# Kernel tuning notes

Measured on AMD Instinct MI355X. Metric: run time of the kernel, lower is better.

Reference implementation:

```python
import jax, jax.numpy as jnp
import numpy as np

H = 8          # n_heads
M = 16         # max_dist
U = 512        # n_units
DH = U // H    # d_head
EPS = 1e-3     # keras LayerNormalization default epsilon
NEG = -2.0**32 + 1.0


def _rel_table(pe, T):
    # pe: [2M+1, DH]; returns [T, T, DH] with rel[i, j] = pe[clip(j - i, -M, M) + M]
    i = jnp.arange(T)
    idx = jnp.clip(i[None, :] - i[:, None], -M, M) + M
    return pe[idx]


def _split_heads(x):
    # [B, T, U] -> [H*B, T, DH]  (head-major, matching tf.concat(tf.split(x, H, 2), 0))
    B, T, _ = x.shape
    return x.reshape(B, T, H, DH).transpose(2, 0, 1, 3).reshape(H * B, T, DH)


def _merge_heads(x, B):
    # [H*B, T, DH] -> [B, T, U]
    T = x.shape[1]
    return x.reshape(H, B, T, DH).transpose(1, 2, 0, 3).reshape(B, T, U)


def setup_inputs() -> dict:
    key = jax.random.key(0)
    ks = jax.random.split(key, 10)
    B, T = 8, 1024
    s = 1.0 / np.sqrt(U)
    inp = {
        'q': jax.random.normal(ks[0], (B, T, U), jnp.float32),
        'k': jax.random.normal(ks[1], (B, T, U), jnp.float32),
        'v': jax.random.normal(ks[2], (B, T, U), jnp.float32),
        'Wq': jax.random.normal(ks[3], (U, U), jnp.float32) * s,
        'bq': jnp.zeros((U,), jnp.float32),
        'Wk': jax.random.normal(ks[4], (U, U), jnp.float32) * s,
        'bk': jnp.zeros((U,), jnp.float32),
        'Wv': jax.random.normal(ks[5], (U, U), jnp.float32) * s,
        'bv': jnp.zeros((U,), jnp.float32),
        'Wo': jax.random.normal(ks[6], (U, U), jnp.float32) * s,
        'bo': jnp.zeros((U,), jnp.float32),
        'gamma': jnp.ones((U,), jnp.float32),
        'beta': jnp.zeros((U,), jnp.float32),
        'pe_k': jax.random.normal(ks[7], (2 * M + 1, DH), jnp.float32) * 0.05,
        'pe_v': jax.random.normal(ks[8], (2 * M + 1, DH), jnp.float32) * 0.05,
    }
    return inp


def reference(q, k, v, Wq, bq, Wk, bk, Wv, bv, Wo, bo, gamma, beta, pe_k, pe_v):
    B, T, _ = q.shape
    relu = jax.nn.relu
    q_emb = relu(q @ Wq + bq)
    k_emb = relu(k @ Wk + bk)
    v_emb = relu(v @ Wv + bv)
    qh = _split_heads(q_emb)   # [HB, T, DH]
    kh = _split_heads(k_emb)
    vh = _split_heads(v_emb)

    attn = jnp.einsum('btd,bsd->bts', qh, kh)
    rel_k = _rel_table(pe_k, T)                       # [T, T, DH]
    attn = attn + jnp.einsum('btd,tsd->bts', qh, rel_k)
    attn = attn / jnp.asarray(DH, attn.dtype) ** 0.5

    causal = jnp.tril(jnp.ones((T, T), jnp.bool_))
    attn = jnp.where(causal[None], attn, jnp.asarray(NEG, attn.dtype))
    w = jax.nn.softmax(attn, axis=-1)

    out = jnp.einsum('bts,bsd->btd', w, vh)
    rel_v = _rel_table(pe_v, T)
    out = out + jnp.einsum('bts,tsd->btd', w, rel_v)

    out = _merge_heads(out, B)                        # [B, T, U]
    out = relu(out @ Wo + bo)
    out = out + q

    mu = jnp.mean(out, axis=-1, keepdims=True)
    var = jnp.mean(jnp.square(out - mu), axis=-1, keepdims=True)
    return (out - mu) * jax.lax.rsqrt(var + EPS) * gamma + beta
```

## Files before the change

### kernel.cpp

```cpp
#include <hip/hip_runtime.h>
#include <hip/hip_bf16.h>

#define T_SEQ 1024
#define U_DIM 512
#define LN_EPS 1e-3f

typedef float  f32x4  __attribute__((ext_vector_type(4)));
typedef short  bf16x8 __attribute__((ext_vector_type(8)));

__device__ __forceinline__ unsigned short f2bf(float f) {
    union { float f; unsigned u; } x; x.f = f;
    unsigned r = x.u + 0x7fffu + ((x.u >> 16) & 1u);
    return (unsigned short)(r >> 16);
}
__device__ __forceinline__ int packbf(float a, float b) {
    return (int)((unsigned)f2bf(a) | ((unsigned)f2bf(b) << 16));
}
__device__ __forceinline__ void async_copy16(void* lds, const void* g) {
    __builtin_amdgcn_global_load_lds((const __attribute__((address_space(1))) void*)g,
                                     (__attribute__((address_space(3))) void*)lds, 16, 0, 0);
}

__global__ __launch_bounds__(256) void prep_wt(const float* __restrict__ W0,
                                               const float* __restrict__ W1,
                                               const float* __restrict__ W2,
                                               const float* __restrict__ W3,
                                               short* __restrict__ wt) {
    __shared__ float Ws[64][65];
    const int z = blockIdx.z;
    const float* W = (z == 0) ? W0 : (z == 1) ? W1 : (z == 2) ? W2 : W3;
    short* Wt = wt + (size_t)z * 262144;
    const int k0 = blockIdx.x * 64, n0 = blockIdx.y * 64;
    const int t = threadIdx.x;
    {
        const int kr = t >> 2, cs = (t & 3) * 16;
        const float4* src = (const float4*)(W + (size_t)(k0 + kr) * 512 + n0 + cs);
#pragma unroll
        for (int i = 0; i < 4; ++i) {
            float4 v = src[i];
            Ws[kr][cs + 4 * i + 0] = v.x;
            Ws[kr][cs + 4 * i + 1] = v.y;
            Ws[kr][cs + 4 * i + 2] = v.z;
            Ws[kr][cs + 4 * i + 3] = v.w;
        }
    }
    __syncthreads();
    {
        const int nr = t >> 2, ks = (t & 3) * 16;
        int4 w0, w1;
        w0.x = packbf(Ws[ks + 0][nr], Ws[ks + 1][nr]);
        w0.y = packbf(Ws[ks + 2][nr], Ws[ks + 3][nr]);
        w0.z = packbf(Ws[ks + 4][nr], Ws[ks + 5][nr]);
        w0.w = packbf(Ws[ks + 6][nr], Ws[ks + 7][nr]);
        w1.x = packbf(Ws[ks + 8][nr], Ws[ks + 9][nr]);
        w1.y = packbf(Ws[ks + 10][nr], Ws[ks + 11][nr]);
        w1.z = packbf(Ws[ks + 12][nr], Ws[ks + 13][nr]);
        w1.w = packbf(Ws[ks + 14][nr], Ws[ks + 15][nr]);
        short* dst = Wt + (size_t)(n0 + nr) * 512 + k0 + ks;
        *(int4*)dst = w0;
        *(int4*)(dst + 8) = w1;
    }
}

template <int AFP32, int OUT>
__global__ __launch_bounds__(256) void gemm_mfma(
        const void* __restrict__ A0, const void* __restrict__ A1, const void* __restrict__ A2,
        const short* __restrict__ Wt0, const short* __restrict__ Wt1, const short* __restrict__ Wt2,
        const float* __restrict__ b0p, const float* __restrict__ b1p, const float* __restrict__ b2p,
        const float* __restrict__ resid,
        void* __restrict__ O0, void* __restrict__ O1, void* __restrict__ O2) {
    __shared__ short As[8192];
    __shared__ short Bs[8192];

    const int z = blockIdx.z;
    const void* Av = (z == 0) ? A0 : (z == 1) ? A1 : A2;
    const short* Wz = (z == 0) ? Wt0 : (z == 1) ? Wt1 : Wt2;
    const float* bz = (z == 0) ? b0p : (z == 1) ? b1p : b2p;
    void* Ov = (z == 0) ? O0 : (z == 1) ? O1 : O2;

    const int tid = threadIdx.x;
    const int m0 = blockIdx.x * 128, n0 = blockIdx.y * 128;
    const int w = tid >> 6, lane = tid & 63;
    const int n15 = lane & 15, g = lane >> 4;
    const int mh = w >> 1, nh = w & 1;

    f32x4 acc[4][4];
#pragma unroll
    for (int i = 0; i < 4; ++i)
#pragma unroll
        for (int j = 0; j < 4; ++j) acc[i][j] = (f32x4){0.f, 0.f, 0.f, 0.f};

    const int am = tid >> 1, akh = tid & 1;

    for (int ck = 0; ck < 8; ++ck) {
        const int k0 = ck * 64;
        if (ck) __syncthreads();

        if (AFP32) {
            const float* asrc = (const float*)Av + (size_t)(m0 + am) * 512 + k0 + akh * 32;
            float4 f[8];
#pragma unroll
            for (int i = 0; i < 8; ++i) f[i] = ((const float4*)asrc)[i];
            short* cell = As + (akh * 8 + (am >> 4)) * 512;
#pragma unroll
            for (int gg = 0; gg < 4; ++gg) {
                int4 wv;
                wv.x = packbf(f[2 * gg].x, f[2 * gg].y);
                wv.y = packbf(f[2 * gg].z, f[2 * gg].w);
                wv.z = packbf(f[2 * gg + 1].x, f[2 * gg + 1].y);
                wv.w = packbf(f[2 * gg + 1].z, f[2 * gg + 1].w);
                *(int4*)(cell + ((am & 15) + 16 * gg) * 8) = wv;
            }
            if (w < 2) {
#pragma unroll
                for (int i = 0; i < 8; ++i) {
                    const int kc = i >> 2, nt = w * 4 + (i & 3);
                    const short* gp = Wz + (size_t)(n0 + nt * 16 + n15) * 512 + k0 + kc * 32 + g * 8;
                    async_copy16(Bs + (kc * 8 + nt) * 512, gp);
                }
            }
        } else {
            if (w < 2) {
#pragma unroll
                for (int i = 0; i < 8; ++i) {
                    const int kc = i >> 2, nt = w * 4 + (i & 3);
                    const short* gp = Wz + (size_t)(n0 + nt * 16 + n15) * 512 + k0 + kc * 32 + g * 8;
                    async_copy16(Bs + (kc * 8 + nt) * 512, gp);
                }
            } else {
#pragma unroll
                for (int i = 0; i < 8; ++i) {
                    const int kc = i >> 2, mt = (w - 2) * 4 + (i & 3);
                    const short* gp = (const short*)Av + (size_t)(m0 + mt * 16 + n15) * 512 + k0 + kc * 32 + g * 8;
                    async_copy16(As + (kc * 8 + mt) * 512, gp);
                }
            }
        }
        __syncthreads();

#pragma unroll
        for (int kc = 0; kc < 2; ++kc) {
            bf16x8 af[4], bf[4];
#pragma unroll
            for (int i = 0; i < 4; ++i)
                af[i] = *(const bf16x8*)(As + (kc * 8 + mh * 4 + i) * 512 + lane * 8);
#pragma unroll
            for (int j = 0; j < 4; ++j)
                bf[j] = *(const bf16x8*)(Bs + (kc * 8 + nh * 4 + j) * 512 + lane * 8);
#pragma unroll
            for (int i = 0; i < 4; ++i)
#pragma unroll
                for (int j = 0; j < 4; ++j)
                    acc[i][j] = __builtin_amdgcn_mfma_f32_16x16x32_bf16(af[i], bf[j], acc[i][j], 0, 0, 0);
        }
    }

    const int mbase = m0 + mh * 64 + g * 4;
    const int nbase = n0 + nh * 64 + n15;
    const bool even = (n15 & 1) == 0;
    float bj[4];
#pragma unroll
    for (int j = 0; j < 4; ++j) bj[j] = bz[nbase + j * 16];

#pragma unroll
    for (int i = 0; i < 4; ++i) {
        const int mrow = mbase + i * 16;
#pragma unroll
        for (int j = 0; j < 4; ++j) {
            const int ncol = nbase + j * 16;
            f32x4 a = acc[i][j];
// ... 31 lines not shown
                    *(float2*)(Oz + (size_t)(mrow + 1) * 512 + ncol) = make_float2(v1 + r1.x, x1 + r1.y);
                } else {
                    float2 r2 = *(const float2*)(resid + (size_t)(mrow + 2) * 512 + ncol - 1);
                    float2 r3 = *(const float2*)(resid + (size_t)(mrow + 3) * 512 + ncol - 1);
                    *(float2*)(Oz + (size_t)(mrow + 2) * 512 + ncol - 1) = make_float2(x2 + r2.x, v2 + r2.y);
                    *(float2*)(Oz + (size_t)(mrow + 3) * 512 + ncol - 1) = make_float2(x3 + r3.x, v3 + r3.y);
                }
            }
        }
    }
}

__global__ __launch_bounds__(256) void attn_mfma(
        const short* __restrict__ qe, const short* __restrict__ ke,
        const short* __restrict__ ve, const float* __restrict__ pe_k,
        const float* __restrict__ pe_v, short* __restrict__ ao) {
    __shared__ short Ks[64 * 72];
    __shared__ short Vt[64 * 72];
    __shared__ float qpeS[128 * 17];
    __shared__ float wsumS[128 * 17];
    __shared__ float alphaS[128];
    __shared__ float lfinS[128];
    __shared__ float pevS[17 * 64];

    const int tid = threadIdx.x;
    const int qt = 7 - (int)blockIdx.x;
    const int hb = blockIdx.y;
    const int h = hb >> 3, b = hb & 7;
    const int t0 = qt * 128;
    const int w = tid >> 6;
    const int lane = tid & 63;
    const int g = lane >> 4;
    const int n15 = lane & 15;
    const int qbase = t0 + w * 32;

    float* qpeW  = qpeS  + w * (32 * 17);
    float* wsumW = wsumS + w * (32 * 17);
    float* alphaW = alphaS + w * 32;
    float* lW = lfinS + w * 32;

    for (int i = tid; i < 17 * 64; i += 256) pevS[i] = pe_v[i];

    bf16x8 Bq[2][2];
#pragma unroll
    for (int nt = 0; nt < 2; ++nt)
#pragma unroll
    for (int kh = 0; kh < 2; ++kh)
        Bq[nt][kh] = *(const bf16x8*)(qe + (size_t)(b * T_SEQ + qbase + nt * 16 + n15) * U_DIM
                                      + h * 64 + kh * 32 + g * 8);

    {
        f32x4 qa[2][2];
#pragma unroll
        for (int mt = 0; mt < 2; ++mt)
#pragma unroll
        for (int nt = 0; nt < 2; ++nt) qa[mt][nt] = (f32x4){0.f, 0.f, 0.f, 0.f};
#pragma unroll
        for (int mt = 0; mt < 2; ++mt)
#pragma unroll
        for (int kh = 0; kh < 2; ++kh) {
            const float* src = pe_k + (mt * 16 + n15) * 64 + kh * 32 + g * 8;
            float4 f0 = *(const float4*)src;
            float4 f1 = *(const float4*)(src + 4);
// ... 4 lines not shown
            fr[6] = (short)f2bf(f1.z); fr[7] = (short)f2bf(f1.w);
#pragma unroll
            for (int nt = 0; nt < 2; ++nt)
                qa[mt][nt] = __builtin_amdgcn_mfma_f32_16x16x32_bf16(fr, Bq[nt][kh], qa[mt][nt], 0, 0, 0);
        }
#pragma unroll
        for (int mt = 0; mt < 2; ++mt)
#pragma unroll
        for (int nt = 0; nt < 2; ++nt)
#pragma unroll
        for (int r = 0; r < 4; ++r) {
            const int ri = mt * 16 + 4 * g + r;
            if (ri <= 16) qpeW[(nt * 16 + n15) * 17 + ri] = qa[mt][nt][r];
        }
    }

    for (int i = lane; i < 32 * 17; i += 64) wsumW[i] = 0.f;

    float m_r[2] = {-3.0e38f, -3.0e38f};
    float l_r[2] = {0.f, 0.f};
    float b0[2]  = {0.f, 0.f};
    f32x4 oacc[2][4];
#pragma unroll
    for (int nt = 0; nt < 2; ++nt)
#pragma unroll
    for (int dt = 0; dt < 4; ++dt) oacc[nt][dt] = (f32x4){0.f, 0.f, 0.f, 0.f};

    const int wqhi = qbase + 31;
    const int send = t0 + 127;

    for (int s0 = 0; s0 <= send; s0 += 64) {
        __syncthreads();
        {
            const int sl = tid >> 2, dseg = (tid & 3) * 16;
            const short* src = ke + (size_t)(b * T_SEQ + s0 + sl) * U_DIM + h * 64 + dseg;
            *(int4*)(Ks + sl * 72 + dseg)     = *(const int4*)src;
            *(int4*)(Ks + sl * 72 + dseg + 8) = *(const int4*)(src + 8);
        }
        {
            const int sp = tid & 31, dbase = (tid >> 5) * 8;
            const short* r0 = ve + (size_t)(b * T_SEQ + s0 + 2 * sp) * U_DIM + h * 64 + dbase;
            const short* r1 = r0 + U_DIM;
            bf16x8 x8 = *(const bf16x8*)r0;
            bf16x8 y8 = *(const bf16x8*)r1;
#pragma unroll
            for (int i = 0; i < 8; ++i) {
                int pv = (int)((unsigned short)x8[i]) | (((int)(unsigned short)y8[i]) << 16);
                *(int*)(Vt + (dbase + i) * 72 + 2 * sp) = pv;
            }
        }
        __syncthreads();

        if (s0 > wqhi) continue;

        int cls[4][2];
#pragma unroll
        for (int mt = 0; mt < 4; ++mt)
#pragma unroll
        for (int nt = 0; nt < 2; ++nt) {
            const int slo = s0 + mt * 16;
            const int qlo = qbase + nt * 16;
            cls[mt][nt] = (slo > qlo + 15) ? 0 : ((slo + 31 < qlo) ? 1 : 2);
        }

        f32x4 c[4][2];
#pragma unroll
        for (int mt = 0; mt < 4; ++mt)
#pragma unroll
        for (int nt = 0; nt < 2; ++nt) c[mt][nt] = (f32x4){0.f, 0.f, 0.f, 0.f};
#pragma unroll
        for (int mt = 0; mt < 4; ++mt) {
            if (cls[mt][0] == 0 && cls[mt][1] == 0) continue;
#pragma unroll
            for (int kh = 0; kh < 2; ++kh) {
                bf16x8 ak = *(const bf16x8*)(Ks + (mt * 16 + n15) * 72 + kh * 32 + g * 8);
#pragma unroll
                for (int nt = 0; nt < 2; ++nt)
                    if (cls[mt][nt])
                        c[mt][nt] = __builtin_amdgcn_mfma_f32_16x16x32_bf16(ak, Bq[nt][kh], c[mt][nt], 0, 0, 0);
            }
        }

        float p[4][2][4];
        float alpha_l[2];
#pragma unroll
        for (int nt = 0; nt < 2; ++nt) {
            const int qg = qbase + nt * 16 + n15;
            const float qpe0 = qpeW[(nt * 16 + n15) * 17];
            float sc[4][4];
            float pmax = -3.0e38f;
#pragma unroll
            for (int mt = 0; mt < 4; ++mt) {
                if (cls[mt][nt] == 0) {
#pragma unroll
                    for (int r = 0; r < 4; ++r) sc[mt][r] = -3.0e38f;
                } else if (cls[mt][nt] == 1) {
#pragma unroll
                    for (int r = 0; r < 4; ++r) {
                        sc[mt][r] = (c[mt][nt][r] + qpe0) * 0.125f;
                        pmax = fmaxf(pmax, sc[mt][r]);
                    }
                } else {
#pragma unroll
                    for (int r = 0; r < 4; ++r) {
                        const int sg = s0 + mt * 16 + 4 * g + r;
                        const int dlt = sg - qg;
                        if (dlt <= 0) {
                            const int ri = (dlt < -16) ? 0 : (dlt + 16);
                            sc[mt][r] = (c[mt][nt][r] + qpeW[(nt * 16 + n15) * 17 + ri]) * 0.125f;
                            pmax = fmaxf(pmax, sc[mt][r]);
                        } else {
                            sc[mt][r] = -3.0e38f;
                        }
                    }
                }
            }
            pmax = fmaxf(pmax, __shfl_xor(pmax, 16, 64));
            pmax = fmaxf(pmax, __shfl_xor(pmax, 32, 64));
            const float mnew = fmaxf(m_r[nt], pmax);
            const float alpha = __expf(m_r[nt] - mnew);
            float psum = 0.f;
#pragma unroll
            for (int mt = 0; mt < 4; ++mt)
#pragma unroll
            for (int r = 0; r < 4; ++r) {
                const float pv = (cls[mt][nt] == 0) ? 0.f : __expf(sc[mt][r] - mnew);
                p[mt][nt][r] = pv;
                psum += pv;
            }
            psum += __shfl_xor(psum, 16, 64);
            psum += __shfl_xor(psum, 32, 64);
            l_r[nt] = l_r[nt] * alpha + psum;
            m_r[nt] = mnew;
            alpha_l[nt] = alpha;
            b0[nt] *= alpha;
        }

        if (g == 0) { alphaW[n15] = alpha_l[0]; alphaW[16 + n15] = alpha_l[1]; }
        for (int i = lane; i < 544; i += 64) wsumW[i] *= alphaW[i / 17];
#pragma unroll
        for (int nt = 0; nt < 2; ++nt) {
            const int qg = qbase + nt * 16 + n15;
#pragma unroll
            for (int mt = 0; mt < 4; ++mt) {
                if (cls[mt][nt] == 1) {
                    b0[nt] += p[mt][nt][0] + p[mt][nt][1] + p[mt][nt][2] + p[mt][nt][3];
                } else if (cls[mt][nt] == 2) {
#pragma unroll
                    for (int r = 0; r < 4; ++r) {
                        const int sg = s0 + mt * 16 + 4 * g + r;
                        const int dlt = sg - qg;
                        if (dlt <= 0) {
                            if (dlt >= -16)
                                atomicAdd(&wsumW[(nt * 16 + n15) * 17 + dlt + 16], p[mt][nt][r]);
                            else
                                b0[nt] += p[mt][nt][r];
                        }
                    }
                }
            }
        }

        int pk01[4][2], pk23[4][2];
#pragma unroll
        for (int mt = 0; mt < 4; ++mt)
#pragma unroll
        for (int nt = 0; nt < 2; ++nt) {
            pk01[mt][nt] = packbf(p[mt][nt][0], p[mt][nt][1]);
            pk23[mt][nt] = packbf(p[mt][nt][2], p[mt][nt][3]);
        }
        const int srcA = ((g & 1) * 2) * 16 + n15;
        const int srcB = srcA + 16;
        const bool selHi = (g >> 1) != 0;
#pragma unroll
        for (int nt = 0; nt < 2; ++nt) {
            float aO[4];
#pragma unroll
            for (int r = 0; r < 4; ++r) aO[r] = alphaW[nt * 16 + 4 * g + r];
#pragma unroll
            for (int dt = 0; dt < 4; ++dt)
#pragma unroll
            for (int r = 0; r < 4; ++r) oacc[nt][dt][r] *= aO[r];
#pragma unroll
            for (int kh = 0; kh < 2; ++kh) {
                if (cls[2 * kh][nt] == 0 && cls[2 * kh + 1][nt] == 0) continue;
                const int a0l = __shfl(pk01[2 * kh][nt], srcA, 64);
                const int a0h = __shfl(pk01[2 * kh + 1][nt], srcA, 64);
                const int a1l = __shfl(pk23[2 * kh][nt], srcA, 64);
                const int a1h = __shfl(pk23[2 * kh + 1][nt], srcA, 64);
                const int a2l = __shfl(pk01[2 * kh][nt], srcB, 64);
                const int a2h = __shfl(pk01[2 * kh + 1][nt], srcB, 64);
                const int a3l = __shfl(pk23[2 * kh][nt], srcB, 64);
                const int a3h = __shfl(pk23[2 * kh + 1][nt], srcB, 64);
                union { int i[4]; bf16x8 v; } au;
                au.i[0] = selHi ? a0h : a0l;
                au.i[1] = selHi ? a1h : a1l;
                au.i[2] = selHi ? a2h : a2l;
                au.i[3] = selHi ? a3h : a3l;
#pragma unroll
                for (int dt = 0; dt < 4; ++dt) {
                    bf16x8 bv = *(const bf16x8*)(Vt + (dt * 16 + n15) * 72 + kh * 32 + g * 8);
                    oacc[nt][dt] = __builtin_amdgcn_mfma_f32_16x16x32_bf16(au.v, bv, oacc[nt][dt], 0, 0, 0);
                }
            }
        }
    }

#pragma unroll
    for (int nt = 0; nt < 2; ++nt) {
        float t = b0[nt];
        t += __shfl_xor(t, 16, 64);
        t += __shfl_xor(t, 32, 64);
        if (g == 0) wsumW[(nt * 16 + n15) * 17] += t;
    }
    if (g == 0) { lW[n15] = l_r[0]; lW[16 + n15] = l_r[1]; }

#pragma unroll
    for (int nt = 0; nt < 2; ++nt)
#pragma unroll
    for (int r = 0; r < 4; ++r) {
        const int ql = nt * 16 + 4 * g + r;
        const int qg = qbase + ql;
        const float linv = 1.0f / lW[ql];
        float w17[17];
#pragma unroll
        for (int ri = 0; ri < 17; ++ri) w17[ri] = wsumW[ql * 17 + ri];
        short* dst = ao + (size_t)(b * T_SEQ + qg) * U_DIM + h * 64 + n15;
#pragma unroll
        for (int dt = 0; dt < 4; ++dt) {
            float relv = 0.f;
#pragma unroll
            for (int ri = 0; ri < 17; ++ri) relv += w17[ri] * pevS[ri * 64 + dt * 16 + n15];
            dst[dt * 16] = (short)f2bf((oacc[nt][dt][r] + relv) * linv);
        }
    }
}

__global__ __launch_bounds__(256) void ln_kernel(float* __restrict__ io,
                                                 const float* __restrict__ gamma,
                                                 const float* __restrict__ beta) {
    const int row = blockIdx.x;
    const int tid = threadIdx.x;
    float* rp = &io[(size_t)row * 512];
    float2 v = *(float2*)&rp[tid * 2];

    float s = v.x + v.y;
#pragma unroll
    for (int off = 32; off > 0; off >>= 1) s += __shfl_down(s, off);

    __shared__ float red[4];
    __shared__ float bc[2];
    const int wid = tid >> 6, lane = tid & 63;
    if (lane == 0) red[wid] = s;
    __syncthreads();
    if (tid == 0) bc[0] = (red[0] + red[1] + red[2] + red[3]) * (1.0f / 512.0f);
    __syncthreads();
    const float mu = bc[0];

    const float d0 = v.x - mu, d1 = v.y - mu;
    float sq = d0 * d0 + d1 * d1;
#pragma unroll
    for (int off = 32; off > 0; off >>= 1) sq += __shfl_down(sq, off);
    if (lane == 0) red[wid] = sq;
    __syncthreads();
    if (tid == 0)
        bc[1] = rsqrtf((red[0] + red[1] + red[2] + red[3]) * (1.0f / 512.0f) + LN_EPS);
    __syncthreads();
    const float rs = bc[1];

    const int c = tid * 2;
    float2 o;
    o.x = d0 * rs * gamma[c] + beta[c];
    o.y = d1 * rs * gamma[c + 1] + beta[c + 1];
    *(float2*)&rp[c] = o;
}

extern "C" void kernel_launch(void* const* d_in, const int* in_sizes, int n_in,
                              void* d_out, int out_size, void* d_ws, size_t ws_size,
                              hipStream_t stream) {
    const float* q     = (const float*)d_in[0];
    const float* k     = (const float*)d_in[1];
    const float* v     = (const float*)d_in[2];
    const float* Wq    = (const float*)d_in[3];
    const float* bq    = (const float*)d_in[4];
    const float* Wk    = (const float*)d_in[5];
    const float* bk    = (const float*)d_in[6];
    const float* Wv    = (const float*)d_in[7];
    const float* bv    = (const float*)d_in[8];
    const float* Wo    = (const float*)d_in[9];
    const float* bo    = (const float*)d_in[10];
    const float* gamma = (const float*)d_in[11];
    const float* beta  = (const float*)d_in[12];
    const float* pe_k  = (const float*)d_in[13];
    const float* pe_v  = (const float*)d_in[14];
    float* out = (float*)d_out;

    char* base = (char*)d_ws;
    short* qe = (short*)(base);
    short* ke = (short*)(base + (((size_t)8) << 20));
    short* ve = (short*)(base + (((size_t)16) << 20));
    short* ao = (short*)(base + (((size_t)24) << 20));
    short* wt = (short*)(base + (((size_t)32) << 20));
    short* wtq = wt, *wtk = wt + 262144, *wtv = wt + 2 * 262144, *wto = wt + 3 * 262144;

    prep_wt<<<dim3(8, 8, 4), 256, 0, stream>>>(Wq, Wk, Wv, Wo, wt);
    gemm_mfma<1, 0><<<dim3(64, 4, 3), 256, 0, stream>>>(
        q, k, v, wtq, wtk, wtv, bq, bk, bv, nullptr, qe, ke, ve);
    attn_mfma<<<dim3(8, 64), 256, 0, stream>>>(qe, ke, ve, pe_k, pe_v, ao);
    gemm_mfma<0, 1><<<dim3(64, 4, 1), 256, 0, stream>>>(
        ao, ao, ao, wto, wto, wto, bo, bo, bo, q, out, out, out);
    ln_kernel<<<dim3(8192), 256, 0, stream>>>(out, gamma, beta);
}
```

Measured before the change: 282.2 us.

## Restructure pipeline: bf16 pre-cast, double-buffered GEMM, split band rel-v kernel, warp LN

After: 273.1 us. 1.03x faster.

```diff
diff --git a/kernel.cpp b/kernel.cpp
--- a/kernel.cpp
+++ b/kernel.cpp
@@ -13,6 +13,10 @@
     unsigned r = x.u + 0x7fffu + ((x.u >> 16) & 1u);
     return (unsigned short)(r >> 16);
 }
+__device__ __forceinline__ float b2f(short s) {
+    union { unsigned u; float f; } x; x.u = ((unsigned)(unsigned short)s) << 16;
+    return x.f;
+}
 __device__ __forceinline__ int packbf(float a, float b) {
     return (int)((unsigned)f2bf(a) | ((unsigned)f2bf(b) << 16));
 }
@@ -21,59 +25,79 @@
                                      (__attribute__((address_space(3))) void*)lds, 16, 0, 0);
 }
 
-__global__ __launch_bounds__(256) void prep_wt(const float* __restrict__ W0,
-                                               const float* __restrict__ W1,
-                                               const float* __restrict__ W2,
-                                               const float* __restrict__ W3,
-                                               short* __restrict__ wt) {
+__global__ __launch_bounds__(256) void prep_all(
+        const float* __restrict__ Wq, const float* __restrict__ Wk,
+        const float* __restrict__ Wv, const float* __restrict__ Wo,
+        short* __restrict__ wt,
+        const float* __restrict__ q, const float* __restrict__ k,
+        const float* __restrict__ v,
+        short* __restrict__ qb, short* __restrict__ kb, short* __restrict__ vb) {
     __shared__ float Ws[64][65];
-    const int z = blockIdx.z;
-    const float* W = (z == 0) ? W0 : (z == 1) ? W1 : (z == 2) ? W2 : W3;
-    short* Wt = wt + (size_t)z * 262144;
-    const int k0 = blockIdx.x * 64, n0 = blockIdx.y * 64;
-    const int t = threadIdx.x;
-    {
-        const int kr = t >> 2, cs = (t & 3) * 16;
-        const float4* src = (const float4*)(W + (size_t)(k0 + kr) * 512 + n0 + cs);
-#pragma unroll
-        for (int i = 0; i < 4; ++i) {
-            float4 v = src[i];
-            Ws[kr][cs + 4 * i + 0] = v.x;
-            Ws[kr][cs + 4 * i + 1] = v.y;
-            Ws[kr][cs + 4 * i + 2] = v.z;
-            Ws[kr][cs + 4 * i + 3] = v.w;
-        }
-    }
-    __syncthreads();
-    {
-        const int nr = t >> 2, ks = (t & 3) * 16;
-        int4 w0, w1;
-        w0.x = packbf(Ws[ks + 0][nr], Ws[ks + 1][nr]);
-        w0.y = packbf(Ws[ks + 2][nr], Ws[ks + 3][nr]);
-        w0.z = packbf(Ws[ks + 4][nr], Ws[ks + 5][nr]);
-        w0.w = packbf(Ws[ks + 6][nr], Ws[ks + 7][nr]);
-        w1.x = packbf(Ws[ks + 8][nr], Ws[ks + 9][nr]);
-        w1.y = packbf(Ws[ks + 10][nr], Ws[ks + 11][nr]);
-        w1.z = packbf(Ws[ks + 12][nr], Ws[ks + 13][nr]);
-        w1.w = packbf(Ws[ks + 14][nr], Ws[ks + 15][nr]);
-        short* dst = Wt + (size_t)(n0 + nr) * 512 + k0 + ks;
-        *(int4*)dst = w0;
-        *(int4*)(dst + 8) = w1;
-    }
-}
-
-template <int AFP32, int OUT>
-__global__ __launch_bounds__(256) void gemm_mfma(
-        const void* __restrict__ A0, const void* __restrict__ A1, const void* __restrict__ A2,
+    const int bid = blockIdx.x, t = threadIdx.x;
+    if (bid < 256) {
+        const int z = bid >> 6, tile = bid & 63;
+        const float* W = (z == 0) ? Wq : (z == 1) ? Wk : (z == 2) ? Wv : Wo;
+        short* Wt = wt + (size_t)z * 262144;
+        const int k0 = (tile >> 3) * 64, n0 = (tile & 7) * 64;
+        {
+            const int kr = t >> 2, cs = (t & 3) * 16;
+            const float4* src = (const float4*)(W + (size_t)(k0 + kr) * 512 + n0 + cs);
+#pragma unroll
+            for (int i = 0; i < 4; ++i) {
+                float4 vv = src[i];
+                Ws[kr][cs + 4 * i + 0] = vv.x;
+                Ws[kr][cs + 4 * i + 1] = vv.y;
+                Ws[kr][cs + 4 * i + 2] = vv.z;
+                Ws[kr][cs + 4 * i + 3] = vv.w;
+            }
+        }
+        __syncthreads();
+        {
+            const int nr = t >> 2, ks = (t & 3) * 16;
+            int4 w0, w1;
+            w0.x = packbf(Ws[ks + 0][nr], Ws[ks + 1][nr]);
+            w0.y = packbf(Ws[ks + 2][nr], Ws[ks + 3][nr]);
+            w0.z = packbf(Ws[ks + 4][nr], Ws[ks + 5][nr]);
+            w0.w = packbf(Ws[ks + 6][nr], Ws[ks + 7][nr]);
+            w1.x = packbf(Ws[ks + 8][nr], Ws[ks + 9][nr]);
+            w1.y = packbf(Ws[ks + 10][nr], Ws[ks + 11][nr]);
+            w1.z = packbf(Ws[ks + 12][nr], Ws[ks + 13][nr]);
+            w1.w = packbf(Ws[ks + 14][nr], Ws[ks + 15][nr]);
+            short* dst = Wt + (size_t)(n0 + nr) * 512 + k0 + ks;
+            *(int4*)dst = w0;
+            *(int4*)(dst + 8) = w1;
+        }
+    } else {
+        const int aid = bid - 256;
+        const int tsr = aid >> 10, chunk = aid & 1023;
+        const float* src = ((tsr == 0) ? q : (tsr == 1) ? k : v) + (size_t)chunk * 4096 + t * 16;
+        short* dst = ((tsr == 0) ? qb : (tsr == 1) ? kb : vb) + (size_t)chunk * 4096 + t * 16;
+        float4 f0 = ((const float4*)src)[0];
+        float4 f1 = ((const float4*)src)[1];
+        float4 f2 = ((const float4*)src)[2];
+        float4 f3 = ((const float4*)src)[3];
+        int4 o0, o1;
+        o0.x = packbf(f0.x, f0.y); o0.y = packbf(f0.z, f0.w);
+        o0.z = packbf(f1.x, f1.y); o0.w = packbf(f1.z, f1.w);
+        o1.x = packbf(f2.x, f2.y); o1.y = packbf(f2.z, f2.w);
+        o1.z = packbf(f3.x, f3.y); o1.w = packbf(f3.z, f3.w);
+        *(int4*)dst = o0;
+        *(int4*)(dst + 8) = o1;
+    }
+}
+
+template <int OUT>
+__global__ __launch_bounds__(256) void gemm_bf16(
+        const short* __restrict__ A0, const short* __restrict__ A1, const short* __restrict__ A2,
         const short* __restrict__ Wt0, const short* __restrict__ Wt1, const short* __restrict__ Wt2,
         const float* __restrict__ b0p, const float* __restrict__ b1p, const float* __restrict__ b2p,
         const float* __restrict__ resid,
         void* __restrict__ O0, void* __restrict__ O1, void* __restrict__ O2) {
-    __shared__ short As[8192];
-    __shared__ short Bs[8192];
+    __shared__ short As[2 * 8192];
+    __shared__ short Bs[2 * 8192];
 
     const int z = blockIdx.z;
-    const void* Av = (z == 0) ? A0 : (z == 1) ? A1 : A2;
+    const short* Az = (z == 0) ? A0 : (z == 1) ? A1 : A2;
     const short* Wz = (z == 0) ? Wt0 : (z == 1) ? Wt1 : Wt2;
     const float* bz = (z == 0) ? b0p : (z == 1) ? b1p : b2p;
     void* Ov = (z == 0) ? O0 : (z == 1) ? O1 : O2;
@@ -90,70 +114,50 @@
 #pragma unroll
         for (int j = 0; j < 4; ++j) acc[i][j] = (f32x4){0.f, 0.f, 0.f, 0.f};
 
-    const int am = tid >> 1, akh = tid & 1;
-
+#define GEMM_STAGE(CK, BUF)                                                              \
+    do {                                                                                 \
+        const int k0s = (CK) * 64;                                                       \
+        short* Ab = As + (BUF) * 8192;                                                   \
+        short* Bb = Bs + (BUF) * 8192;                                                   \
+        if (w < 2) {                                                                     \
+            _Pragma("unroll")                                                            \
+            for (int i = 0; i < 8; ++i) {                                                \
+                const int kc = i >> 2, nt = w * 4 + (i & 3);                             \
+                const short* gp = Wz + (size_t)(n0 + nt * 16 + n15) * 512 + k0s + kc * 32 + g * 8; \
+                async_copy16(Bb + (kc * 8 + nt) * 512, gp);                              \
+            }                                                                            \
+        } else {                                                                         \
+            _Pragma("unroll")                                                            \
+            for (int i = 0; i < 8; ++i) {                                                \
+                const int kc = i >> 2, mt = (w - 2) * 4 + (i & 3);                       \
+                const short* gp = Az + (size_t)(m0 + mt * 16 + n15) * 512 + k0s + kc * 32 + g * 8; \
+                async_copy16(Ab + (kc * 8 + mt) * 512, gp);                              \
+            }                                                                            \
+        }                                                                                \
+    } while (0)
+
+    GEMM_STAGE(0, 0);
     for (int ck = 0; ck < 8; ++ck) {
-        const int k0 = ck * 64;
-        if (ck) __syncthreads();
-
-        if (AFP32) {
-            const float* asrc = (const float*)Av + (size_t)(m0 + am) * 512 + k0 + akh * 32;
-            float4 f[8];
-#pragma unroll
-            for (int i = 0; i < 8; ++i) f[i] = ((const float4*)asrc)[i];
-            short* cell = As + (akh * 8 + (am >> 4)) * 512;
-#pragma unroll
-            for (int gg = 0; gg < 4; ++gg) {
-                int4 wv;
-                wv.x = packbf(f[2 * gg].x, f[2 * gg].y);
-                wv.y = packbf(f[2 * gg].z, f[2 * gg].w);
-                wv.z = packbf(f[2 * gg + 1].x, f[2 * gg + 1].y);
-                wv.w = packbf(f[2 * gg + 1].z, f[2 * gg + 1].w);
-                *(int4*)(cell + ((am & 15) + 16 * gg) * 8) = wv;
-            }
-            if (w < 2) {
-#pragma unroll
-                for (int i = 0; i < 8; ++i) {
-                    const int kc = i >> 2, nt = w * 4 + (i & 3);
-                    const short* gp = Wz + (size_t)(n0 + nt * 16 + n15) * 512 + k0 + kc * 32 + g * 8;
-                    async_copy16(Bs + (kc * 8 + nt) * 512, gp);
-                }
-            }
-        } else {
-            if (w < 2) {
-#pragma unroll
-                for (int i = 0; i < 8; ++i) {
-                    const int kc = i >> 2, nt = w * 4 + (i & 3);
-                    const short* gp = Wz + (size_t)(n0 + nt * 16 + n15) * 512 + k0 + kc * 32 + g * 8;
-                    async_copy16(Bs + (kc * 8 + nt) * 512, gp);
-                }
-            } else {
-#pragma unroll
-                for (int i = 0; i < 8; ++i) {
-                    const int kc = i >> 2, mt = (w - 2) * 4 + (i & 3);
-                    const short* gp = (const short*)Av + (size_t)(m0 + mt * 16 + n15) * 512 + k0 + kc * 32 + g * 8;
-                    async_copy16(As + (kc * 8 + mt) * 512, gp);
-                }
-            }
-        }
         __syncthreads();
-
+        if (ck < 7) GEMM_STAGE(ck + 1, (ck + 1) & 1);
+        const int buf = ck & 1;
 #pragma unroll
         for (int kc = 0; kc < 2; ++kc) {
-            bf16x8 af[4], bf[4];
+            bf16x8 af[4], bfv[4];
 #pragma unroll
             for (int i = 0; i < 4; ++i)
-                af[i] = *(const bf16x8*)(As + (kc * 8 + mh * 4 + i) * 512 + lane * 8);
+                af[i] = *(const bf16x8*)(As + buf * 8192 + (kc * 8 + mh * 4 + i) * 512 + lane * 8);
 #pragma unroll
             for (int j = 0; j < 4; ++j)
-                bf[j] = *(const bf16x8*)(Bs + (kc * 8 + nh * 4 + j) * 512 + lane * 8);
+                bfv[j] = *(const bf16x8*)(Bs + buf * 8192 + (kc * 8 + nh * 4 + j) * 512 + lane * 8);
 #pragma unroll
             for (int i = 0; i < 4; ++i)
 #pragma unroll
                 for (int j = 0; j < 4; ++j)
-                    acc[i][j] = __builtin_amdgcn_mfma_f32_16x16x32_bf16(af[i], bf[j], acc[i][j], 0, 0, 0);
-        }
-    }
+                    acc[i][j] = __builtin_amdgcn_mfma_f32_16x16x32_bf16(af[i], bfv[j], acc[i][j], 0, 0, 0);
+        }
+    }
+#undef GEMM_STAGE
 
     const int mbase = m0 + mh * 64 + g * 4;
     const int nbase = n0 + nh * 64 + n15;
@@ -215,39 +219,31 @@
 __global__ __launch_bounds__(256) void attn_mfma(
         const short* __restrict__ qe, const short* __restrict__ ke,
         const short* __restrict__ ve, const float* __restrict__ pe_k,
-        const float* __restrict__ pe_v, short* __restrict__ ao) {
-    __shared__ short Ks[64 * 72];
-    __shared__ short Vt[64 * 72];
-    __shared__ float qpeS[128 * 17];
-    __shared__ float wsumS[128 * 17];
-    __shared__ float alphaS[128];
-    __shared__ float lfinS[128];
-    __shared__ float pevS[17 * 64];
+        float* __restrict__ ml, short* __restrict__ ao) {
+    __shared__ short Kc[2 * 4096];
+    __shared__ short Vt[2 * 4608];
+    __shared__ float qpeS[4 * 32 * 17];
 
     const int tid = threadIdx.x;
     const int qt = 7 - (int)blockIdx.x;
     const int hb = blockIdx.y;
     const int h = hb >> 3, b = hb & 7;
     const int t0 = qt * 128;
-    const int w = tid >> 6;
-    const int lane = tid & 63;
-    const int g = lane >> 4;
-    const int n15 = lane & 15;
-    const int qbase = t0 + w * 32;
-
-    float* qpeW  = qpeS  + w * (32 * 17);
-    float* wsumW = wsumS + w * (32 * 17);
-    float* alphaW = alphaS + w * 32;
-    float* lW = lfinS + w * 32;
-
-    for (int i = tid; i < 17 * 64; i += 256) pevS[i] = pe_v[i];
+    const int w = tid >> 6, lane = tid & 63;
+    const int g = lane >> 4, n15 = lane & 15;
+    const int qn[2] = {t0 + w * 16, t0 + (7 - w) * 16};
+    const int wqhi = qn[1] + 15;
+    const int nsteps = (t0 + 128) >> 6;
+    const int sp = tid & 31, dbase = (tid >> 5) * 8;
+
+    float* qpeW = qpeS + w * (32 * 17);
 
     bf16x8 Bq[2][2];
 #pragma unroll
     for (int nt = 0; nt < 2; ++nt)
 #pragma unroll
     for (int kh = 0; kh < 2; ++kh)
-        Bq[nt][kh] = *(const bf16x8*)(qe + (size_t)(b * T_SEQ + qbase + nt * 16 + n15) * U_DIM
+        Bq[nt][kh] = *(const bf16x8*)(qe + (size_t)(b * T_SEQ + qn[nt] + n15) * U_DIM
                                       + h * 64 + kh * 32 + g * 8);
 
     {
@@ -282,265 +278,328 @@
             if (ri <= 16) qpeW[(nt * 16 + n15) * 17 + ri] = qa[mt][nt][r];
         }
     }
-
-    for (int i = lane; i < 32 * 17; i += 64) wsumW[i] = 0.f;
+    const float qpe0r[2] = { qpeW[(n15) * 17], qpeW[(16 + n15) * 17] };
 
     float m_r[2] = {-3.0e38f, -3.0e38f};
     float l_r[2] = {0.f, 0.f};
-    float b0[2]  = {0.f, 0.f};
     f32x4 oacc[2][4];
 #pragma unroll
     for (int nt = 0; nt < 2; ++nt)
 #pragma unroll
     for (int dt = 0; dt < 4; ++dt) oacc[nt][dt] = (f32x4){0.f, 0.f, 0.f, 0.f};
 
-    const int wqhi = qbase + 31;
-    const int send = t0 + 127;
-
-    for (int s0 = 0; s0 <= send; s0 += 64) {
+    {
+#pragma unroll
+        for (int j = 0; j < 2; ++j) {
+            const int cc = 2 * w + j, kh = cc >> 2, mt = cc & 3;
+            const short* gp = ke + (size_t)(b * T_SEQ + mt * 16 + n15) * U_DIM + h * 64 + kh * 32 + g * 8;
+            async_copy16(Kc + cc * 512, gp);
+        }
+        const short* r0 = ve + (size_t)(b * T_SEQ + 2 * sp) * U_DIM + h * 64 + dbase;
+        bf16x8 vx = *(const bf16x8*)r0, vy = *(const bf16x8*)(r0 + U_DIM);
+#pragma unroll
+        for (int ii = 0; ii < 8; ++ii) {
+            int pv = (int)((unsigned short)vx[ii]) | (((int)(unsigned short)vy[ii]) << 16);
+            *(int*)(Vt + (dbase + ii) * 72 + 2 * sp) = pv;
+        }
+    }
+
+    for (int i = 0; i < nsteps; ++i) {
+        const int s0 = i << 6;
+        const int cbuf = i & 1, nbuf = cbuf ^ 1;
+        const bool hasnext = (i + 1) < nsteps;
+        bf16x8 vx, vy;
         __syncthreads();
-        {
-            const int sl = tid >> 2, dseg = (tid & 3) * 16;
-            const short* src = ke + (size_t)(b * T_SEQ + s0 + sl) * U_DIM + h * 64 + dseg;
-            *(int4*)(Ks + sl * 72 + dseg)     = *(const int4*)src;
-            *(int4*)(Ks + sl * 72 + dseg + 8) = *(const int4*)(src + 8);
-        }
-        {
-            const int sp = tid & 31, dbase = (tid >> 5) * 8;
-            const short* r0 = ve + (size_t)(b * T_SEQ + s0 + 2 * sp) * U_DIM + h * 64 + dbase;
-            const short* r1 = r0 + U_DIM;
-            bf16x8 x8 = *(const bf16x8*)r0;
-            bf16x8 y8 = *(const bf16x8*)r1;
-#pragma unroll
-            for (int i = 0; i < 8; ++i) {
-                int pv = (int)((unsigned short)x8[i]) | (((int)(unsigned short)y8[i]) << 16);
-                *(int*)(Vt + (dbase + i) * 72 + 2 * sp) = pv;
-            }
-        }
-        __syncthreads();
-
-        if (s0 > wqhi) continue;
-
-        int cls[4][2];
-#pragma unroll
-        for (int mt = 0; mt < 4; ++mt)
-#pragma unroll
-        for (int nt = 0; nt < 2; ++nt) {
-            const int slo = s0 + mt * 16;
-            const int qlo = qbase + nt * 16;
-            cls[mt][nt] = (slo > qlo + 15) ? 0 : ((slo + 31 < qlo) ? 1 : 2);
-        }
-
-        f32x4 c[4][2];
-#pragma unroll
-        for (int mt = 0; mt < 4; ++mt)
-#pragma unroll
-        for (int nt = 0; nt < 2; ++nt) c[mt][nt] = (f32x4){0.f, 0.f, 0.f, 0.f};
-#pragma unroll
-        for (int mt = 0; mt < 4; ++mt) {
-            if (cls[mt][0] == 0 && cls[mt][1] == 0) continue;
-#pragma unroll
-            for (int kh = 0; kh < 2; ++kh) {
-                bf16x8 ak = *(const bf16x8*)(Ks + (mt * 16 + n15) * 72 + kh * 32 + g * 8);
-#pragma unroll
-                for (int nt = 0; nt < 2; ++nt)
-                    if (cls[mt][nt])
-                        c[mt][nt] = __builtin_amdgcn_mfma_f32_16x16x32_bf16(ak, Bq[nt][kh], c[mt][nt], 0, 0, 0);
-            }
-        }
-
-        float p[4][2][4];
-        float alpha_l[2];
-#pragma unroll
-        for (int nt = 0; nt < 2; ++nt) {
-            const int qg = qbase + nt * 16 + n15;
-            const float qpe0 = qpeW[(nt * 16 + n15) * 17];
-            float sc[4][4];
-            float pmax = -3.0e38f;
+        if (hasnext) {
+            const int sn = s0 + 64;
+#pragma unroll
+            for (int j = 0; j < 2; ++j) {
+                const int cc = 2 * w + j, kh = cc >> 2, mt = cc & 3;
+                const short* gp = ke + (size_t)(b * T_SEQ + sn + mt * 16 + n15) * U_DIM + h * 64 + kh * 32 + g * 8;
+                async_copy16(Kc + nbuf * 4096 + cc * 512, gp);
+            }
+            const short* r0 = ve + (size_t)(b * T_SEQ + sn + 2 * sp) * U_DIM + h * 64 + dbase;
+            vx = *(const bf16x8*)r0;
+            vy = *(const bf16x8*)(r0 + U_DIM);
+        }
+
+        if (s0 <= wqhi) {
+            int cls[4][2];
+#pragma unroll
+            for (int mt = 0; mt < 4; ++mt)
+#pragma unroll
+            for (int nt = 0; nt < 2; ++nt) {
+                const int slo = s0 + mt * 16;
+                const int qlo = qn[nt];
+                cls[mt][nt] = (slo > qlo + 15) ? 0 : ((slo + 31 < qlo) ? 1 : 2);
+            }
+
+            f32x4 c[4][2];
+#pragma unroll
+            for (int mt = 0; mt < 4; ++mt)
+#pragma unroll
+            for (int nt = 0; nt < 2; ++nt) c[mt][nt] = (f32x4){0.f, 0.f, 0.f, 0.f};
 #pragma unroll
             for (int mt = 0; mt < 4; ++mt) {
-                if (cls[mt][nt] == 0) {
-#pragma unroll
-                    for (int r = 0; r < 4; ++r) sc[mt][r] = -3.0e38f;
-                } else if (cls[mt][nt] == 1) {
-#pragma unroll
-                    for (int r = 0; r < 4; ++r) {
-                        sc[mt][r] = (c[mt][nt][r] + qpe0) * 0.125f;
-                        pmax = fmaxf(pmax, sc[mt][r]);
-                    }
-                } else {
-#pragma unroll
-                    for (int r = 0; r < 4; ++r) {
-                        const int sg = s0 + mt * 16 + 4 * g + r;
-                        const int dlt = sg - qg;
-                        if (dlt <= 0) {
-                            const int ri = (dlt < -16) ? 0 : (dlt + 16);
-                            sc[mt][r] = (c[mt][nt][r] + qpeW[(nt * 16 + n15) * 17 + ri]) * 0.125f;
+                if (cls[mt][0] == 0 && cls[mt][1] == 0) continue;
+#pragma unroll
+                for (int kh = 0; kh < 2; ++kh) {
+                    bf16x8 ak = *(const bf16x8*)(Kc + cbuf * 4096 + (kh * 4 + mt) * 512 + lane * 8);
+#pragma unroll
+                    for (int nt = 0; nt < 2; ++nt)
+                        if (cls[mt][nt])
+                            c[mt][nt] = __builtin_amdgcn_mfma_f32_16x16x32_bf16(ak, Bq[nt][kh], c[mt][nt], 0, 0, 0);
+                }
+            }
+
+            float p[4][2][4];
+            float alpha_l[2];
+#pragma unroll
+            for (int nt = 0; nt < 2; ++nt) {
+                const int qg = qn[nt] + n15;
+                float sc[4][4];
+                float pmax = -3.0e38f;
+#pragma unroll
+                for (int mt = 0; mt < 4; ++mt) {
+                    if (cls[mt][nt] == 0) {
+#pragma unroll
+                        for (int r = 0; r < 4; ++r) sc[mt][r] = -3.0e38f;
+                    } else if (cls[mt][nt] == 1) {
+#pragma unroll
+                        for (int r = 0; r < 4; ++r) {
+                            sc[mt][r] = (c[mt][nt][r] + qpe0r[nt]) * 0.125f;
                             pmax = fmaxf(pmax, sc[mt][r]);
-                        } else {
-                            sc[mt][r] = -3.0e38f;
+                        }
+                    } else {
+#pragma unroll
+                        for (int r = 0; r < 4; ++r) {
+                            const int sg = s0 + mt * 16 + 4 * g + r;
+                            const int dlt = sg - qg;
+                            if (dlt <= 0) {
+                                const int ri = (dlt < -16) ? 0 : (dlt + 16);
+                                sc[mt][r] = (c[mt][nt][r] + qpeW[(nt * 16 + n15) * 17 + ri]) * 0.125f;
+                                pmax = fmaxf(pmax, sc[mt][r]);
+                            } else {
+                                sc[mt][r] = -3.0e38f;
+                            }
                         }
                     }
                 }
-            }
-            pmax = fmaxf(pmax, __shfl_xor(pmax, 16, 64));
-            pmax = fmaxf(pmax, __shfl_xor(pmax, 32, 64));
-            const float mnew = fmaxf(m_r[nt], pmax);
-            const float alpha = __expf(m_r[nt] - mnew);
-            float psum = 0.f;
+                pmax = fmaxf(pmax, __shfl_xor(pmax, 16, 64));
+                pmax = fmaxf(pmax, __shfl_xor(pmax, 32, 64));
+                const float mnew = fmaxf(m_r[nt], pmax);
+                const float alpha = __expf(m_r[nt] - mnew);
+                float psum = 0.f;
+#pragma unroll
+                for (int mt = 0; mt < 4; ++mt)
+#pragma unroll
+                for (int r = 0; r < 4; ++r) {
+                    const float pv = (cls[mt][nt] == 0) ? 0.f : __expf(sc[mt][r] - mnew);
+                    p[mt][nt][r] = pv;
+                    psum += pv;
+                }
+                psum += __shfl_xor(psum, 16, 64);
+                psum += __shfl_xor(psum, 32, 64);
+                l_r[nt] = l_r[nt] * alpha + psum;
+                m_r[nt] = mnew;
+                alpha_l[nt] = alpha;
+            }
+
+            int pk01[4][2], pk23[4][2];
 #pragma unroll
             for (int mt = 0; mt < 4; ++mt)
 #pragma unroll
-            for (int r = 0; r < 4; ++r) {
-                const float pv = (cls[mt][nt] == 0) ? 0.f : __expf(sc[mt][r] - mnew);
-                p[mt][nt][r] = pv;
-                psum += pv;
-            }
-            psum += __shfl_xor(psum, 16, 64);
-            psum += __shfl_xor(psum, 32, 64);
-            l_r[nt] = l_r[nt] * alpha + psum;
-            m_r[nt] = mnew;
-            alpha_l[nt] = alpha;
-            b0[nt] *= alpha;
-        }
-
-        if (g == 0) { alphaW[n15] = alpha_l[0]; alphaW[16 + n15] = alpha_l[1]; }
-        for (int i = lane; i < 544; i += 64) wsumW[i] *= alphaW[i / 17];
-#pragma unroll
-        for (int nt = 0; nt < 2; ++nt) {
-            const int qg = qbase + nt * 16 + n15;
-#pragma unroll
-            for (int mt = 0; mt < 4; ++mt) {
-                if (cls[mt][nt] == 1) {
-                    b0[nt] += p[mt][nt][0] + p[mt][nt][1] + p[mt][nt][2] + p[mt][nt][3];
-                } else if (cls[mt][nt] == 2) {
-#pragma unroll
-                    for (int r = 0; r < 4; ++r) {
-                        const int sg = s0 + mt * 16 + 4 * g + r;
-                        const int dlt = sg - qg;
-                        if (dlt <= 0) {
-                            if (dlt >= -16)
-                                atomicAdd(&wsumW[(nt * 16 + n15) * 17 + dlt + 16], p[mt][nt][r]);
-                            else
-                                b0[nt] += p[mt][nt][r];
-                        }
+            for (int nt = 0; nt < 2; ++nt) {
+                pk01[mt][nt] = packbf(p[mt][nt][0], p[mt][nt][1]);
+                pk23[mt][nt] = packbf(p[mt][nt][2], p[mt][nt][3]);
+            }
+            const int srcA = ((g & 1) * 2) * 16 + n15;
+            const int srcB = srcA + 16;
+            const bool selHi = (g >> 1) != 0;
+#pragma unroll
+            for (int nt = 0; nt < 2; ++nt) {
+                float aO[4];
+#pragma unroll
+                for (int r = 0; r < 4; ++r) aO[r] = __shfl(alpha_l[nt], 4 * g + r, 64);
+#pragma unroll
+                for (int dt = 0; dt < 4; ++dt)
+#pragma unroll
+                for (int r = 0; r < 4; ++r) oacc[nt][dt][r] *= aO[r];
+#pragma unroll
+                for (int kh = 0; kh < 2; ++kh) {
+                    if (cls[2 * kh][nt] == 0 && cls[2 * kh + 1][nt] == 0) continue;
+                    const int a0l = __shfl(pk01[2 * kh][nt], srcA, 64);
+                    const int a0h = __shfl(pk01[2 * kh + 1][nt], srcA, 64);
+                    const int a1l = __shfl(pk23[2 * kh][nt], srcA, 64);
+                    const int a1h = __shfl(pk23[2 * kh + 1][nt], srcA, 64);
+                    const int a2l = __shfl(pk01[2 * kh][nt], srcB, 64);
+                    const int a2h = __shfl(pk01[2 * kh + 1][nt], srcB, 64);
+                    const int a3l = __shfl(pk23[2 * kh][nt], srcB, 64);
+                    const int a3h = __shfl(pk23[2 * kh + 1][nt], srcB, 64);
+                    union { int i[4]; bf16x8 v; } au;
+                    au.i[0] = selHi ? a0h : a0l;
+                    au.i[1] = selHi ? a1h : a1l;
+                    au.i[2] = selHi ? a2h : a2l;
+                    au.i[3] = selHi ? a3h : a3l;
+#pragma unroll
+                    for (int dt = 0; dt < 4; ++dt) {
+                        bf16x8 bv = *(const bf16x8*)(Vt + cbuf * 4608 + (dt * 16 + n15) * 72 + kh * 32 + g * 8);
+                        oacc[nt][dt] = __builtin_amdgcn_mfma_f32_16x16x32_bf16(au.v, bv, oacc[nt][dt], 0, 0, 0);
                     }
                 }
             }
         }
 
-        int pk01[4][2], pk23[4][2];
-#pragma unroll
-        for (int mt = 0; mt < 4; ++mt)
-#pragma unroll
-        for (int nt = 0; nt < 2; ++nt) {
-            pk01[mt][nt] = packbf(p[mt][nt][0], p[mt][nt][1]);
-            pk23[mt][nt] = packbf(p[mt][nt][2], p[mt][nt][3]);
-        }
-        const int srcA = ((g & 1) * 2) * 16 + n15;
-        const int srcB = srcA + 16;
-        const bool selHi = (g >> 1) != 0;
-#pragma unroll
-        for (int nt = 0; nt < 2; ++nt) {
-            float aO[4];
-#pragma unroll
-            for (int r = 0; r < 4; ++r) aO[r] = alphaW[nt * 16 + 4 * g + r];
-#pragma unroll
-            for (int dt = 0; dt < 4; ++dt)
-#pragma unroll
-            for (int r = 0; r < 4; ++r) oacc[nt][dt][r] *= aO[r];
-#pragma unroll
-            for (int kh = 0; kh < 2; ++kh) {
-                if (cls[2 * kh][nt] == 0 && cls[2 * kh + 1][nt] == 0) continue;
-                const int a0l = __shfl(pk01[2 * kh][nt], srcA, 64);
-                const int a0h = __shfl(pk01[2 * kh + 1][nt], srcA, 64);
-                const int a1l = __shfl(pk23[2 * kh][nt], srcA, 64);
-                const int a1h = __shfl(pk23[2 * kh + 1][nt], srcA, 64);
-                const int a2l = __shfl(pk01[2 * kh][nt], srcB, 64);
-                const int a2h = __shfl(pk01[2 * kh + 1][nt], srcB, 64);
-                const int a3l = __shfl(pk23[2 * kh][nt], srcB, 64);
-                const int a3h = __shfl(pk23[2 * kh + 1][nt], srcB, 64);
-                union { int i[4]; bf16x8 v; } au;
-                au.i[0] = selHi ? a0h : a0l;
-                au.i[1] = selHi ? a1h : a1l;
-                au.i[2] = selHi ? a2h : a2l;
-                au.i[3] = selHi ? a3h : a3l;
-#pragma unroll
-                for (int dt = 0; dt < 4; ++dt) {
-                    bf16x8 bv = *(const bf16x8*)(Vt + (dt * 16 + n15) * 72 + kh * 32 + g * 8);
-                    oacc[nt][dt] = __builtin_amdgcn_mfma_f32_16x16x32_bf16(au.v, bv, oacc[nt][dt], 0, 0, 0);
-                }
+        if (hasnext) {
+#pragma unroll
+            for (int ii = 0; ii < 8; ++ii) {
+                int pv = (int)((unsigned short)vx[ii]) | (((int)(unsigned short)vy[ii]) << 16);
+                *(int*)(Vt + nbuf * 4608 + (dbase + ii) * 72 + 2 * sp) = pv;
             }
         }
     }
 
 #pragma unroll
     for (int nt = 0; nt < 2; ++nt) {
-        float t = b0[nt];
-        t += __shfl_xor(t, 16, 64);
-        t += __shfl_xor(t, 32, 64);
-        if (g == 0) wsumW[(nt * 16 + n15) * 17] += t;
-    }
-    if (g == 0) { lW[n15] = l_r[0]; lW[16 + n15] = l_r[1]; }
-
+        if (g == 0) {
+            float2 v2 = make_float2(m_r[nt], l_r[nt]);
+            *(float2*)(ml + ((size_t)hb * T_SEQ + qn[nt] + n15) * 2) = v2;
+        }
+    }
 #pragma unroll
     for (int nt = 0; nt < 2; ++nt)
 #pragma unroll
     for (int r = 0; r < 4; ++r) {
-        const int ql = nt * 16 + 4 * g + r;
-        const int qg = qbase + ql;
-        const float linv = 1.0f / lW[ql];
-        float w17[17];
-#pragma unroll
-        for (int ri = 0; ri < 17; ++ri) w17[ri] = wsumW[ql * 17 + ri];
+        const float lq = __shfl(l_r[nt], 4 * g + r, 64);
+        const float linv = 1.0f / lq;
+        const int qg = qn[nt] + 4 * g + r;
         short* dst = ao + (size_t)(b * T_SEQ + qg) * U_DIM + h * 64 + n15;
 #pragma unroll
-        for (int dt = 0; dt < 4; ++dt) {
-            float relv = 0.f;
-#pragma unroll
-            for (int ri = 0; ri < 17; ++ri) relv += w17[ri] * pevS[ri * 64 + dt * 16 + n15];
-            dst[dt * 16] = (short)f2bf((oacc[nt][dt][r] + relv) * linv);
-        }
-    }
+        for (int dt = 0; dt < 4; ++dt)
+            dst[dt * 16] = (short)f2bf(oacc[nt][dt][r] * linv);
+    }
+}
+
+__global__ __launch_bounds__(256) void band_relv(
+        const short* __restrict__ qe, const short* __restrict__ ke,
+        const float* __restrict__ pe_k, const float* __restrict__ pe_v,
+        const float* __restrict__ ml, short* __restrict__ ao) {
+    __shared__ float pek[17 * 64];
+    __shared__ float pev[17 * 64];
+    const int tb = blockIdx.x, hb = blockIdx.y;
+    const int h = hb >> 3, b = hb & 7;
+    const int tid = threadIdx.x;
+    for (int i = tid; i < 17 * 64; i += 256) {
+        pek[i] = b2f((short)f2bf(pe_k[i]));
+        pev[i] = pe_v[i];
+    }
+    __syncthreads();
+
+    const int t = tb * 64 + (tid >> 2);
+    const int p = (tid & 3) * 16;
+    const short* qp = qe + (size_t)(b * T_SEQ + t) * U_DIM + h * 64 + p;
+    bf16x8 qa = *(const bf16x8*)qp, qb2 = *(const bf16x8*)(qp + 8);
+    float qv[16];
+#pragma unroll
+    for (int i = 0; i < 8; ++i) { qv[i] = b2f(qa[i]); qv[8 + i] = b2f(qb2[i]); }
+
+    float dots[17];
+#pragma unroll
+    for (int ri = 0; ri < 17; ++ri) {
+        const int s = t - 16 + ri;
+        float acc = 0.f;
+        if (s >= 0) {
+            const short* kp = ke + (size_t)(b * T_SEQ + s) * U_DIM + h * 64 + p;
+            bf16x8 ka = *(const bf16x8*)kp, kb2 = *(const bf16x8*)(kp + 8);
+#pragma unroll
+            for (int d = 0; d < 8; ++d) {
+                acc += qv[d] * b2f(ka[d]);
+                acc += qv[8 + d] * b2f(kb2[d]);
+            }
+#pragma unroll
+            for (int d = 0; d < 16; ++d) acc += qv[d] * pek[ri * 64 + p + d];
+        }
+        dots[ri] = acc;
+    }
+#pragma unroll
+    for (int ri = 0; ri < 17; ++ri) {
+        dots[ri] += __shfl_xor(dots[ri], 1, 64);
+        dots[ri] += __shfl_xor(dots[ri], 2, 64);
+    }
+
+    const float2 mlv = *(const float2*)(ml + ((size_t)hb * T_SEQ + t) * 2);
+    const float m = mlv.x, linv = 1.0f / mlv.y;
+    float wv[17];
+    float wsum = 0.f;
+#pragma unroll
+    for (int ri = 0; ri < 17; ++ri) {
+        const int s = t - 16 + ri;
+        const float wr = (s >= 0) ? __expf(dots[ri] * 0.125f - m) * linv : 0.f;
+        wv[ri] = wr;
+        wsum += wr;
+    }
+    wv[0] += 1.0f - wsum;
+
+    float relv[16];
+#pragma unroll
+    for (int d = 0; d < 16; ++d) relv[d] = 0.f;
+#pragma unroll
+    for (int ri = 0; ri < 17; ++ri)
+#pragma unroll
+        for (int d = 0; d < 16; ++d) relv[d] += wv[ri] * pev[ri * 64 + p + d];
+
+    short* op = ao + (size_t)(b * T_SEQ + t) * U_DIM + h * 64 + p;
+    bf16x8 a0 = *(const bf16x8*)op, a1 = *(const bf16x8*)(op + 8);
+    int4 o0, o1;
+    o0.x = packbf(b2f(a0[0]) + relv[0],  b2f(a0[1]) + relv[1]);
+    o0.y = packbf(b2f(a0[2]) + relv[2],  b2f(a0[3]) + relv[3]);
+    o0.z = packbf(b2f(a0[4]) + relv[4],  b2f(a0[5]) + relv[5]);
+    o0.w = packbf(b2f(a0[6]) + relv[6],  b2f(a0[7]) + relv[7]);
+    o1.x = packbf(b2f(a1[0]) + relv[8],  b2f(a1[1]) + relv[9]);
+    o1.y = packbf(b2f(a1[2]) + relv[10], b2f(a1[3]) + relv[11]);
+    o1.z = packbf(b2f(a1[4]) + relv[12], b2f(a1[5]) + relv[13]);
+    o1.w = packbf(b2f(a1[6]) + relv[14], b2f(a1[7]) + relv[15]);
+    *(int4*)op = o0;
+    *(int4*)(op + 8) = o1;
 }
 
 __global__ __launch_bounds__(256) void ln_kernel(float* __restrict__ io,
                                                  const float* __restrict__ gamma,
                                                  const float* __restrict__ beta) {
-    const int row = blockIdx.x;
-    const int tid = threadIdx.x;
-    float* rp = &io[(size_t)row * 512];
-    float2 v = *(float2*)&rp[tid * 2];
-
-    float s = v.x + v.y;
-#pragma unroll
-    for (int off = 32; off > 0; off >>= 1) s += __shfl_down(s, off);
-
-    __shared__ float red[4];
-    __shared__ float bc[2];
-    const int wid = tid >> 6, lane = tid & 63;
-    if (lane == 0) red[wid] = s;
-    __syncthreads();
-    if (tid == 0) bc[0] = (red[0] + red[1] + red[2] + red[3]) * (1.0f / 512.0f);
-    __syncthreads();
-    const float mu = bc[0];
-
-    const float d0 = v.x - mu, d1 = v.y - mu;
-    float sq = d0 * d0 + d1 * d1;
-#pragma unroll
-    for (int off = 32; off > 0; off >>= 1) sq += __shfl_down(sq, off);
-    if (lane == 0) red[wid] = sq;
-    __syncthreads();
-    if (tid == 0)
-        bc[1] = rsqrtf((red[0] + red[1] + red[2] + red[3]) * (1.0f / 512.0f) + LN_EPS);
-    __syncthreads();
-    const float rs = bc[1];
-
-    const int c = tid * 2;
-    float2 o;
-    o.x = d0 * rs * gamma[c] + beta[c];
-    o.y = d1 * rs * gamma[c + 1] + beta[c + 1];
-    *(float2*)&rp[c] = o;
+    const int row = blockIdx.x * 4 + (threadIdx.x >> 6);
+    const int lane = threadIdx.x & 63;
+    float* rp = io + (size_t)row * 512 + lane * 8;
+    float4 a = *(const float4*)rp;
+    float4 c = *(const float4*)(rp + 4);
+    float v[8] = {a.x, a.y, a.z, a.w, c.x, c.y, c.z, c.w};
+
+    float s = v[0] + v[1] + v[2] + v[3] + v[4] + v[5] + v[6] + v[7];
+#pragma unroll
+    for (int off = 1; off < 64; off <<= 1) s += __shfl_xor(s, off, 64);
+    const float mu = s * (1.0f / 512.0f);
+
+    float sq = 0.f;
+#pragma unroll
+    for (int i = 0; i < 8; ++i) { v[i] -= mu; sq += v[i] * v[i]; }
+#pragma unroll
+    for (int off = 1; off < 64; off <<= 1) sq += __shfl_xor(sq, off, 64);
+    const float rs = rsqrtf(sq * (1.0f / 512.0f) + LN_EPS);
+
+    const float4 g0 = *(const float4*)(gamma + lane * 8);
+    const float4 g1 = *(const float4*)(gamma + lane * 8 + 4);
+    const float4 b0 = *(const float4*)(beta + lane * 8);
+    const float4 b1 = *(const float4*)(beta + lane * 8 + 4);
+    float4 o0, o1;
+    o0.x = v[0] * rs * g0.x + b0.x;
+    o0.y = v[1] * rs * g0.y + b0.y;
+    o0.z = v[2] * rs * g0.z + b0.z;
+    o0.w = v[3] * rs * g0.w + b0.w;
+    o1.x = v[4] * rs * g1.x + b1.x;
+    o1.y = v[5] * rs * g1.y + b1.y;
+    o1.z = v[6] * rs * g1.z + b1.z;
+    o1.w = v[7] * rs * g1.w + b1.w;
+    *(float4*)rp = o0;
+    *(float4*)(rp + 4) = o1;
 }
 
 extern "C" void kernel_launch(void* const* d_in, const int* in_sizes, int n_in,
@@ -564,18 +623,23 @@
     float* out = (float*)d_out;
 
     char* base = (char*)d_ws;
-    short* qe = (short*)(base);
-    short* ke = (short*)(base + (((size_t)8) << 20));
-    short* ve = (short*)(base + (((size_t)16) << 20));
-    short* ao = (short*)(base + (((size_t)24) << 20));
-    short* wt = (short*)(base + (((size_t)32) << 20));
+    short* qb = (short*)(base);
+    short* kb = (short*)(base + (((size_t)8) << 20));
+    short* vb = (short*)(base + (((size_t)16) << 20));
+    short* qe = (short*)(base + (((size_t)24) << 20));
+    short* ke = (short*)(base + (((size_t)32) << 20));
+    short* ve = (short*)(base + (((size_t)40) << 20));
+    short* ao = (short*)(base + (((size_t)48) << 20));
+    short* wt = (short*)(base + (((size_t)56) << 20));
+    float* ml = (float*)(base + (((size_t)58) << 20));
     short* wtq = wt, *wtk = wt + 262144, *wtv = wt + 2 * 262144, *wto = wt + 3 * 262144;
 
-    prep_wt<<<dim3(8, 8, 4), 256, 0, stream>>>(Wq, Wk, Wv, Wo, wt);
-    gemm_mfma<1, 0><<<dim3(64, 4, 3), 256, 0, stream>>>(
-        q, k, v, wtq, wtk, wtv, bq, bk, bv, nullptr, qe, ke, ve);
-    attn_mfma<<<dim3(8, 64), 256, 0, stream>>>(qe, ke, ve, pe_k, pe_v, ao);
-    gemm_mfma<0, 1><<<dim3(64, 4, 1), 256, 0, stream>>>(
+    prep_all<<<dim3(3328), 256, 0, stream>>>(Wq, Wk, Wv, Wo, wt, q, k, v, qb, kb, vb);
+    gemm_bf16<0><<<dim3(64, 4, 3), 256, 0, stream>>>(
+        qb, kb, vb, wtq, wtk, wtv, bq, bk, bv, nullptr, qe, ke, ve);
+    attn_mfma<<<dim3(8, 64), 256, 0, stream>>>(qe, ke, ve, pe_k, ml, ao);
+    band_relv<<<dim3(16, 64), 256, 0, stream>>>(qe, ke, pe_k, pe_v, ml, ao);
+    gemm_bf16<1><<<dim3(64, 4, 1), 256, 0, stream>>>(
         ao, ao, ao, wto, wto, wto, bo, bo, bo, q, out, out, out);
-    ln_kernel<<<dim3(8192), 256, 0, stream>>>(out, gamma, beta);
-}
+    ln_kernel<<<dim3(2048), 256, 0, stream>>>(out, gamma, beta);
+}
```
